# Optimization experiments

Measured on AMD Instinct MI355X. Metric: run time of the kernel, lower is better.

## Reference

```python
import jax, jax.numpy as jnp
import numpy as np
from jax import lax

SUB, NSUB, FRAME, COND, FEAT, PEMB = 40, 4, 160, 256, 20, 64
B, NB_FRAMES = 64, 100
T = NB_FRAMES + 4  # two valid k=3 convs drop 4 frames


def setup_inputs() -> dict:
    keys = iter(jax.random.split(jax.random.key(0), 40))
    def W(shape, fan_in):
        return jax.random.normal(next(keys), shape, jnp.float32) / np.float32(np.sqrt(fan_in))
    z = lambda *s: jnp.zeros(s, jnp.float32)
    inp = {
        'features': jax.random.normal(next(keys), (B, T, FEAT), jnp.float32),
        'period': jax.random.randint(next(keys), (B, T), 32, 256, jnp.int32),
        'nb_frames': NB_FRAMES,
        'rand_shift': jax.random.uniform(next(keys), (B, 1), jnp.float32),
        'pembed': 0.1 * jax.random.normal(next(keys), (256, PEMB), jnp.float32),
        'fd1_w': W((FEAT + PEMB, COND), FEAT + PEMB), 'fd1_b': z(COND),
        'conv1_w': W((COND, COND, 3), 3 * COND), 'conv1_b': z(COND),
        'conv2_w': W((COND, COND, 3), 3 * COND), 'conv2_b': z(COND),
        'fd2_w': W((COND, COND), COND), 'fd2_b': z(COND),
        'sd1_w': W((3 * SUB + COND, COND), 3 * SUB + COND), 'sd1_b': z(COND),
        'sd2_w': W((COND, COND), COND), 'sd2_b': z(COND),
        'g1_wi': W((COND, 3 * COND), COND), 'g1_bi': z(3 * COND),
        'g1_wh': W((COND, 3 * COND), COND), 'g1_bh': z(3 * COND),
        'g2_wi': W((COND, 3 * COND), COND), 'g2_bi': z(3 * COND),
        'g2_wh': W((COND, 3 * COND), COND), 'g2_bh': z(3 * COND),
        'g3_wi': W((COND, 3 * COND), COND), 'g3_bi': z(3 * COND),
        'g3_wh': W((COND, 3 * COND), COND), 'g3_bh': z(3 * COND),
        'out_w': W((COND, SUB), COND), 'out_b': z(SUB),
    }
    return inp


def _gru(x, h, wi, bi, wh, bh):
    # torch GRUCell gate order: r, z, n
    gi = x @ wi + bi
    gh = h @ wh + bh
    i_r, i_z, i_n = jnp.split(gi, 3, axis=1)
    h_r, h_z, h_n = jnp.split(gh, 3, axis=1)
    r = jax.nn.sigmoid(i_r + h_r)
    zt = jax.nn.sigmoid(i_z + h_z)
    n = jnp.tanh(i_n + r * h_n)
    return (1.0 - zt) * n + zt * h


def _conv1d_valid(x, w, b):
    # x: (B, C, T), w: (O, I, 3)
    y = lax.conv_general_dilated(x, w, (1,), 'VALID', dimension_numbers=('NCH', 'OIH', 'NCH'))
    return y + b[None, :, None]


def _forward(features, rand_shift, pembed, fd1_w, fd1_b, conv1_w, conv1_b, conv2_w, conv2_b,
             fd2_w, fd2_b, sd1_w, sd1_b, sd2_w, sd2_b,
             g1_wi, g1_bi, g1_wh, g1_bh, g2_wi, g2_bi, g2_wh, g2_bh, g3_wi, g3_bi, g3_wh, g3_bh,
             out_w, out_b, period, nb_frames):
    b = features.shape[0]
    two_pi = np.float32(2.0 * np.pi)
    # --- phase embedding (gen_phase_embedding on period[:, 3:-1]) ---
    p = period[:, 3:-1].astype(jnp.float32)              # (B, nb_frames)
    w0 = two_pi / p
    w0_shift = jnp.concatenate([two_pi * rand_shift / FRAME, w0[:, :-1]], axis=1)
    cum_phase = FRAME * jnp.cumsum(w0_shift, axis=1)     # (B, nb_frames)
    fine = w0[:, :, None] * jnp.arange(FRAME, dtype=jnp.float32)
    embed = (cum_phase[:, :, None] + fine).reshape(b, nb_frames * NSUB, SUB)
    phase_real = jnp.cos(embed)
    phase_imag = jnp.sin(embed)
    # --- conditioning network ---
    pe = pembed[period]                                  # (B, T, PEMB)
    t = jnp.tanh(jnp.concatenate([features, pe], axis=-1) @ fd1_w + fd1_b)
    x = t.transpose(0, 2, 1)                             # (B, COND, T)
    x = jnp.tanh(_conv1d_valid(x, conv1_w, conv1_b))
    x = jnp.tanh(_conv1d_valid(x, conv2_w, conv2_b))
    cond = jnp.tanh(x.transpose(0, 2, 1) @ fd2_w + fd2_b)  # (B, T-4, COND)
    cond_steps = jnp.repeat(cond[:, :nb_frames], NSUB, axis=1)  # (B, steps, COND)
    xs = (cond_steps.transpose(1, 0, 2), phase_real.transpose(1, 0, 2), phase_imag.transpose(1, 0, 2))
    h0 = jnp.zeros((b, COND), features.dtype)
    prev0 = jnp.zeros((b, SUB), features.dtype)

    def step(carry, inp):
        prev, h1, h2, h3 = carry
        c, pr, pi = inp
        tt = jnp.tanh(jnp.concatenate([c, prev, pr, pi], axis=1) @ sd1_w + sd1_b)
        tt = jnp.tanh(tt @ sd2_w + sd2_b)
        h1 = _gru(tt, h1, g1_wi, g1_bi, g1_wh, g1_bh)
        h2 = _gru(h1, h2, g2_wi, g2_bi, g2_wh, g2_bh)
        h3 = _gru(h2, h3, g3_wi, g3_bi, g3_wh, g3_bh)
        out = jnp.tanh(h3 @ out_w + out_b)
        return (out, h1, h2, h3), out

    (_, h1, h2, h3), outs = lax.scan(step, (prev0, h0, h0, h0), xs)
    sig = outs.transpose(1, 0, 2).reshape(b, -1)         # (B, nb_frames*FRAME)
    return sig, (h1, h2, h3)


def reference(features, period, nb_frames, rand_shift, pembed, fd1_w, fd1_b, conv1_w, conv1_b,
              conv2_w, conv2_b, fd2_w, fd2_b, sd1_w, sd1_b, sd2_w, sd2_b,
              g1_wi, g1_bi, g1_wh, g1_bh, g2_wi, g2_bi, g2_wh, g2_bh, g3_wi, g3_bi, g3_wh, g3_bh,
              out_w, out_b):
    return _forward(features, rand_shift, pembed, fd1_w, fd1_b, conv1_w, conv1_b, conv2_w, conv2_b,
                    fd2_w, fd2_b, sd1_w, sd1_b, sd2_w, sd2_b,
                    g1_wi, g1_bi, g1_wh, g1_bh, g2_wi, g2_bi, g2_wh, g2_bh,
                    g3_wi, g3_bi, g3_wh, g3_bh, out_w, out_b, period, nb_frames)
```

## Files before the change

kernel.cpp:

```cpp
#include <hip/hip_runtime.h>
#include <hip/hip_bf16.h>
#include <math.h>

#define B_ 64
#define T_ 104
#define FEAT_ 20
#define PEMB_ 64
#define COND_ 256
#define SUB_ 40
#define NBF_ 100
#define STEPS_ 400

typedef short short8 __attribute__((ext_vector_type(8)));
typedef float floatx4 __attribute__((ext_vector_type(4)));
typedef unsigned int uintx4 __attribute__((ext_vector_type(4)));

__device__ inline unsigned short f2bf(float x){
  unsigned int u = __float_as_uint(x);
  unsigned int r = (u + 0x7fffu + ((u >> 16) & 1u)) >> 16;
  return (unsigned short)r;
}
__device__ inline float fast_tanh(float x){
  float e = __expf(2.f*x);
  return 1.f - 2.f*__builtin_amdgcn_rcpf(e + 1.f);
}
__device__ inline float fast_sigm(float x){
  return __builtin_amdgcn_rcpf(1.f + __expf(-x));
}
__device__ inline floatx4 mfma16(short8 a, short8 b, floatx4 c){
  return __builtin_amdgcn_mfma_f32_16x16x32_bf16(a, b, c, 0, 0, 0);
}
__device__ inline unsigned long long ld_coh_u64(const unsigned long long* p){
  return __hip_atomic_load(p, __ATOMIC_RELAXED, __HIP_MEMORY_SCOPE_AGENT);
}
__device__ inline void st_coh_u32(unsigned int* p, unsigned int v){
  __hip_atomic_store(p, v, __ATOMIC_RELAXED, __HIP_MEMORY_SCOPE_AGENT);
}

template<int STRIDE, int GCOFF>
__device__ inline void poll_stage(const unsigned int* __restrict__ src, char* dst,
                                  unsigned tgt, int tid){
  int c0 = tid, c1 = tid + 256;
  int r0 = c0 >> 5, g0 = c0 & 31;
  int r1 = c1 >> 5, g1 = c1 & 31;
  const unsigned long long* p0 = (const unsigned long long*)src + (r0*128 + g0*4);
  const unsigned long long* p1 = (const unsigned long long*)src + (r1*128 + g1*4);
  unsigned long long w[8];
  for (;;){
    #pragma unroll
    for (int u = 0; u < 4; ++u) w[u]   = ld_coh_u64(p0 + u);
    #pragma unroll
    for (int u = 0; u < 4; ++u) w[4+u] = ld_coh_u64(p1 + u);
    unsigned mt = 0xFFFFu;
    #pragma unroll
    for (int u = 0; u < 8; ++u){
      unsigned t0 = (unsigned)(w[u] >> 16) & 0xFFFFu;
      unsigned t1 = (unsigned)(w[u] >> 48);
      mt = min(mt, min(t0, t1));
    }
    if (__all((int)(mt >= tgt))) break;
    __builtin_amdgcn_s_sleep(1);
  }
  unsigned int pk0[4], pk1[4];
  #pragma unroll
  for (int u = 0; u < 4; ++u){
    pk0[u] = ((unsigned int)w[u]   & 0xFFFFu) | ((unsigned int)(w[u]   >> 32) << 16);
    pk1[u] = ((unsigned int)w[4+u] & 0xFFFFu) | ((unsigned int)(w[4+u] >> 32) << 16);
  }
  uintx4 v0 = {pk0[0], pk0[1], pk0[2], pk0[3]};
  uintx4 v1 = {pk1[0], pk1[1], pk1[2], pk1[3]};
  *(uintx4*)(dst + (size_t)(r0*STRIDE + ((GCOFF + g0) ^ (r0 & 7)))*16) = v0;
  *(uintx4*)(dst + (size_t)(r1*STRIDE + ((GCOFF + g1) ^ (r1 & 7)))*16) = v1;
}

__global__ void k_phase(const int* __restrict__ period, const float* __restrict__ rshift,
                        float* __restrict__ pr, float* __restrict__ pi){
  int b = blockIdx.x;
  __shared__ float cumf[NBF_], w0f[NBF_];
  if (threadIdx.x == 0){
    double acc = 2.0*M_PI*(double)rshift[b];
    for (int f = 0; f < NBF_; ++f){
      double w0 = 2.0*M_PI/(double)period[b*T_ + 3 + f];
      cumf[f] = (float)fmod(acc, 2.0*M_PI);
      w0f[f] = (float)w0;
      acc += 160.0*w0;
    }
  }
  __syncthreads();
  for (int e = threadIdx.x; e < NBF_*160; e += blockDim.x){
    int f = e/160, j = e - f*160;
    float ph = cumf[f] + w0f[f]*(float)j;
    int s = f*4 + j/40, u = j%40;
    pr[((size_t)b*STEPS_ + s)*SUB_ + u] = cosf(ph);
    pi[((size_t)b*STEPS_ + s)*SUB_ + u] = sinf(ph);
  }
}

__global__ void k_prep(const float* __restrict__ c1w, const float* __restrict__ c2w,
                       float* __restrict__ w1t, float* __restrict__ w2t,
                       unsigned int* __restrict__ msg){
  size_t tid = (size_t)blockIdx.x*blockDim.x + threadIdx.x;
  size_t nt = (size_t)gridDim.x*blockDim.x;
  for (size_t e = tid; e < 131072; e += nt) st_coh_u32(msg + e, 0u);
  for (size_t e = tid; e < 768u*256u; e += nt){
    int kk = (int)(e >> 8), o = (int)(e & 255);
    int i = kk & 255, kc = kk >> 8;
    w1t[e] = c1w[(size_t)o*768 + i*3 + kc];
    w2t[e] = c2w[(size_t)o*768 + i*3 + kc];
  }
}

template<int MODE>
__global__ __launch_bounds__(256) void k_gemm(
    const float* __restrict__ a0, const float* __restrict__ a1, const float* __restrict__ a2,
    const int* __restrict__ ip,
    const float* __restrict__ Bm, const float* __restrict__ bias, float* __restrict__ C)
{
  constexpr int KT = (MODE==0) ? 6 : (MODE==1||MODE==2) ? 48 : (MODE==3) ? 16 : 21;
  __shared__ float As[16][68];
  __shared__ float Bs[16][68];
  int tid = threadIdx.x;
  int m0 = blockIdx.x*64, n0 = blockIdx.y*64;
  int tx = tid & 15, ty = tid >> 4;
  float acc[4][4] = {};
  int am = m0 + (tid >> 2);
  int akq = (tid & 3)*4;
  int bk = tid >> 4;
  int bn4 = (tid & 15)*4;

  for (int kt = 0; kt < KT; ++kt){
    int kbase = kt*16;
    float av[4];
    {
      int k0 = kbase + akq;
      if constexpr (MODE==0){
        if (k0 < 20){
          const float* p = a0 + (size_t)am*FEAT_ + k0;
          #pragma unroll
          for (int u=0;u<4;++u) av[u] = p[u];
        } else if (k0 < 84){
          const float* p = a1 + (size_t)ip[am]*PEMB_ + (k0-20);
          #pragma unroll
          for (int u=0;u<4;++u) av[u] = p[u];
        } else { av[0]=av[1]=av[2]=av[3]=0.f; }
      } else if constexpr (MODE==1){
        int b = am/102, t2 = am - b*102;
        int i = k0 & 255, kc = k0 >> 8;
        const float* p = a0 + ((size_t)(b*T_ + t2 + kc))*COND_ + i;
        #pragma unroll
        for (int u=0;u<4;++u) av[u] = p[u];
      } else if constexpr (MODE==2){
        int b = am/100, t2 = am - b*100;
        int i = k0 & 255, kc = k0 >> 8;
        const float* p = a0 + ((size_t)(b*102 + t2 + kc))*COND_ + i;
        #pragma unroll
        for (int u=0;u<4;++u) av[u] = p[u];
      } else if constexpr (MODE==3){
        const float* p = a0 + (size_t)am*COND_ + k0;
        #pragma unroll
        for (int u=0;u<4;++u) av[u] = p[u];
      } else {
        int b = am/400, s = am - b*400;
        const float* p;
        if (k0 < 256)      p = a0 + ((size_t)(b*100 + (s>>2)))*COND_ + k0;
        else if (k0 < 296) p = a1 + ((size_t)(b*400 + s))*SUB_ + (k0-256);
        else               p = a2 + ((size_t)(b*400 + s))*SUB_ + (k0-296);
        #pragma unroll
        for (int u=0;u<4;++u) av[u] = p[u];
      }
    }
    float bv[4];
    {
      int kB = kbase + bk;
      if constexpr (MODE==0){
        if (kB < 84){
          const float* p = Bm + (size_t)kB*256 + n0 + bn4;
          #pragma unroll
          for (int u=0;u<4;++u) bv[u] = p[u];
        } else { bv[0]=bv[1]=bv[2]=bv[3]=0.f; }
      } else if constexpr (MODE==4){
        int krow = (kB < 256) ? kB : kB + 40;
        const float* p = Bm + (size_t)krow*256 + n0 + bn4;
        #pragma unroll
        for (int u=0;u<4;++u) bv[u] = p[u];
      } else {
        const float* p = Bm + (size_t)kB*256 + n0 + bn4;
        #pragma unroll
        for (int u=0;u<4;++u) bv[u] = p[u];
      }
    }
    #pragma unroll
    for (int u=0;u<4;++u) As[akq+u][tid>>2] = av[u];
    #pragma unroll
    for (int u=0;u<4;++u) Bs[bk][bn4+u] = bv[u];
    __syncthreads();
    #pragma unroll
    for (int k = 0; k < 16; ++k){
      float a4[4], b4[4];
      #pragma unroll
      for (int i=0;i<4;++i) a4[i] = As[k][ty*4+i];
      #pragma unroll
      for (int j=0;j<4;++j) b4[j] = Bs[k][tx*4+j];
      #pragma unroll
      for (int i=0;i<4;++i)
        #pragma unroll
        for (int j=0;j<4;++j)
          acc[i][j] += a4[i]*b4[j];
    }
    __syncthreads();
  }
  #pragma unroll
  for (int i=0;i<4;++i){
    int m = m0 + ty*4 + i;
    #pragma unroll
    for (int j=0;j<4;++j){
      int n = n0 + tx*4 + j;
      float v = acc[i][j] + bias[n];
      if constexpr (MODE == 4){
        int b = m/400, s = m - b*400;
        C[((size_t)s*64 + b)*256 + n] = v;
      } else {
        C[(size_t)m*256 + n] = fast_tanh(v);
      }
    }
  }
}

__global__ __launch_bounds__(256, 1) void k_scan(
  const float* __restrict__ sd1_w, const float* __restrict__ sd2_w, const float* __restrict__ sd2_b,
  const float* __restrict__ g1_wi, const float* __restrict__ g1_bi, const float* __restrict__ g1_wh, const float* __restrict__ g1_bh,
  const float* __restrict__ g2_wi, const float* __restrict__ g2_bi, const float* __restrict__ g2_wh, const float* __restrict__ g2_bh,
  const float* __restrict__ g3_wi, const float* __restrict__ g3_bi, const float* __restrict__ g3_wh, const float* __restrict__ g3_bh,
  const float* __restrict__ out_w, const float* __restrict__ out_b,
  const float* __restrict__ tt1p,
  unsigned int* __restrict__ tt2buf, unsigned int* __restrict__ h1buf,
  unsigned int* __restrict__ h2buf, unsigned int* __restrict__ h3buf,
  float* __restrict__ out)
{
  __shared__ __align__(16) char smem[65536];
  int tid = threadIdx.x;
  int lane = tid & 63, wave = tid >> 6;
  int q = lane >> 4, nI = lane & 15;
  int bI = blockIdx.x;
  int g = bI >> 6, rr = bI & 63;
  int set = rr >> 4, sl = rr & 15;
  int b0 = g*16;

  if (set == 0){
    char* outwF = smem;
    char* sd1p0 = smem + 24576;
    char* sd1p1 = smem + 40960;
    char* sd2F  = smem + 45056;
    char* stage = smem + 53248;
    char* prevl = smem + 61440;
    int col1 = sl*16 + nI;

    for (int t = wave; t < 24; t += 4){
      int nt = t >> 3, kk = t & 7;
      int c = nt*16 + nI;
      unsigned short v[8];
      #pragma unroll
      for (int j = 0; j < 8; ++j){
        int k = kk*32 + q*8 + j;
        v[j] = (c < 40) ? f2bf(out_w[(size_t)k*40 + c]) : (unsigned short)0;
      }
      *(short8*)(outwF + (t*64 + lane)*16) = *(short8*)v;
    }
    for (int t = wave; t < 16; t += 4){
      unsigned short v[8];
      #pragma unroll
      for (int j = 0; j < 8; ++j){
        int k = q*8 + j;
        v[j] = f2bf(sd1_w[(size_t)(256+k)*256 + t*16 + nI]);
      }
      *(short8*)(sd1p0 + (t*64 + lane)*16) = *(short8*)v;
    }
    {
      int nt = tid >> 4, ln = tid & 15;
      unsigned short v[8];
      #pragma unroll
      for (int j = 0; j < 8; ++j)
        v[j] = f2bf(sd1_w[(size_t)(256+32+j)*256 + nt*16 + ln]);
      *(short8*)(sd1p1 + tid*16) = *(short8*)v;
    }
    for (int t = wave; t < 8; t += 4){
      unsigned short v[8];
      #pragma unroll
      for (int j = 0; j < 8; ++j){
        int k = t*32 + q*8 + j;
        v[j] = f2bf(sd2_w[(size_t)k*256 + col1]);
      }
      *(short8*)(sd2F + (t*64 + lane)*16) = *(short8*)v;
    }
    for (int e = tid; e < 16*72; e += 256) *(unsigned short*)(prevl + e*2) = 0;
    float bout = 0.f;
    if (wave < 3){ int c = wave*16 + nI; if (c < 40) bout = out_b[c]; }
    float bsd2 = sd2_b[col1];
    __syncthreads();

    for (int s = 0; s <= STEPS_; ++s){
      float t1r[16];
      if (s < STEPS_){
        const float* tb = tt1p + ((size_t)s*64 + b0)*256;
        #pragma unroll
        for (int ii = 0; ii < 4; ++ii){
          int c = (wave*4 + ii)*16 + nI;
          #pragma unroll
          for (int i = 0; i < 4; ++i)
            t1r[ii*4+i] = tb[(q*4+i)*256 + c];
        }
      }
      if (s > 0){
        const unsigned int* h3s = h3buf + ((size_t)((s+1)&1)*4 + g)*4096;
        poll_stage<32,0>(h3s, stage, (unsigned)s, tid);
        __syncthreads();
        if (wave < 3){
          floatx4 acc = {0.f,0.f,0.f,0.f};
          #pragma unroll
          for (int kk = 0; kk < 8; ++kk){
            short8 a = *(const short8*)(stage + (nI*32 + ((kk*4+q) ^ (nI & 7)))*16);
            short8 b = *(const short8*)(outwF + ((wave*8+kk)*64 + lane)*16);
            acc = mfma16(a, b, acc);
          }
          int c = wave*16 + nI;
          #pragma unroll
          for (int i = 0; i < 4; ++i){
            int row = q*4 + i;
            float pv = (c < 40) ? fast_tanh(acc[i] + bout) : 0.f;
            *(unsigned short*)(prevl + (row*72 + c)*2) = f2bf(pv);
            if (sl == 0 && c < 40)
              out[(size_t)(b0+row)*16000 + (size_t)(s-1)*40 + c] = pv;
          }
        }
      }
      if (s == STEPS_) break;
      __syncthreads();
      #pragma unroll
      for (int ii = 0; ii < 4; ++ii){
        int nt = wave*4 + ii;
        floatx4 acc = {0.f,0.f,0.f,0.f};
        short8 a0v = *(const short8*)(prevl + nI*144 + q*16);
        short8 b0v = *(const short8*)(sd1p0 + (nt*64 + lane)*16);
        acc = mfma16(a0v, b0v, acc);
        short8 a1v = *(const short8*)(prevl + nI*144 + 64 + q*16);
        short8 b1v = {0,0,0,0,0,0,0,0};
        if (q == 0) b1v = *(const short8*)(sd1p1 + (nt*16 + nI)*16);
        acc = mfma16(a1v, b1v, acc);
        int c = nt*16 + nI;
        #pragma unroll
        for (int i = 0; i < 4; ++i){
          int row = q*4 + i;
          float tv = fast_tanh(acc[i] + t1r[ii*4+i]);
          int gc = c >> 3;
          *(unsigned short*)(stage + (row*32 + (gc ^ (row & 7)))*16 + (c & 7)*2) = f2bf(tv);
        }
      }
      __syncthreads();
      if (wave == 0){
        floatx4 acc = {0.f,0.f,0.f,0.f};
        #pragma unroll
        for (int kk = 0; kk < 8; ++kk){
          short8 a = *(const short8*)(stage + (nI*32 + ((kk*4+q) ^ (nI & 7)))*16);
          short8 b = *(const short8*)(sd2F + (kk*64 + lane)*16);
          acc = mfma16(a, b, acc);
        }
        unsigned int* t2 = tt2buf + ((size_t)(s&1)*4 + g)*4096;
        unsigned int tg = (unsigned)(s+1) << 16;
        #pragma unroll
        for (int i = 0; i < 4; ++i){
          int row = q*4 + i;
          st_coh_u32(&t2[row*256 + col1], tg | (unsigned)f2bf(fast_tanh(acc[i] + bsd2)));
        }
      }
      __syncthreads();
    }
  } else {
    int gi_ = set - 1;
    const float* wi = (gi_==0) ? g1_wi : (gi_==1) ? g2_wi : g3_wi;
    const float* wh = (gi_==0) ? g1_wh : (gi_==1) ? g2_wh : g3_wh;
    const float* bi = (gi_==0) ? g1_bi : (gi_==1) ? g2_bi : g3_bi;
    const float* bh = (gi_==0) ? g1_bh : (gi_==1) ? g2_bh : g3_bh;
    unsigned int* hOut = (gi_==0) ? h1buf : (gi_==1) ? h2buf : h3buf;
    const unsigned int* xBase = (gi_==0) ? tt2buf : (gi_==1) ? h1buf : h2buf;
    char* wlds  = smem;
    char* stage = smem + 49152;
    int hc0 = sl*16;

    for (int t = wave; t < 48; t += 4){
      unsigned short v[8];
      #pragma unroll
      for (int j = 0; j < 8; ++j){
        float w;
        if (t < 32){
          int k512 = (t & 15)*32 + q*8 + j;
          int col = ((t < 16) ? 0 : 256) + hc0 + nI;
          w = (k512 < 256) ? wi[(size_t)k512*768 + col] : wh[(size_t)(k512-256)*768 + col];
        } else if (t < 40){
          int k = (t-32)*32 + q*8 + j;
          w = wi[(size_t)k*768 + 512 + hc0 + nI];
        } else {
          int k = (t-40)*32 + q*8 + j;
          w = wh[(size_t)k*768 + 512 + hc0 + nI];
        }
        v[j] = f2bf(w);
      }
      *(short8*)(wlds + (t*64 + lane)*16) = *(short8*)v;
    }
    int erow = tid >> 4, ecol = tid & 15;
    int cg = hc0 + ecol;
    float br  = bi[cg] + bh[cg];
    float bz  = bi[256+cg] + bh[256+cg];
    float bin = bi[512+cg];
    float bhn = bh[512+cg];
    float hstate = 0.f;
    __syncthreads();

    for (int s = 0; s < STEPS_; ++s){
      const unsigned int* hs = hOut + ((size_t)((s+1)&1)*4 + g)*4096;
      poll_stage<64,32>(hs, stage, (unsigned)s, tid);
      __syncthreads();
      floatx4 acc = {0.f,0.f,0.f,0.f};
      if (wave < 2){
        int tb = wave*16;
        #pragma unroll
        for (int kt = 8; kt < 16; ++kt){
          short8 a = *(const short8*)(stage + (nI*64 + ((kt*4+q) ^ (nI & 7)))*16);
          short8 b = *(const short8*)(wlds + ((tb+kt)*64 + lane)*16);
          acc = mfma16(a, b, acc);
        }
      } else if (wave == 3){
        #pragma unroll
        for (int kt = 0; kt < 8; ++kt){
          short8 a = *(const short8*)(stage + (nI*64 + ((32 + kt*4+q) ^ (nI & 7)))*16);
          short8 b = *(const short8*)(wlds + ((40+kt)*64 + lane)*16);
          acc = mfma16(a, b, acc);
        }
      }
      const unsigned int* xs = xBase + ((size_t)(s&1)*4 + g)*4096;
      poll_stage<64,0>(xs, stage, (unsigned)(s+1), tid);
      __syncthreads();
      if (wave < 2){
        int tb = wave*16;
        #pragma unroll
        for (int kt = 0; kt < 8; ++kt){
          short8 a = *(const short8*)(stage + (nI*64 + ((kt*4+q) ^ (nI & 7)))*16);
          short8 b = *(const short8*)(wlds + ((tb+kt)*64 + lane)*16);
          acc = mfma16(a, b, acc);
        }
      } else if (wave == 2){
        #pragma unroll
        for (int kt = 0; kt < 8; ++kt){
          short8 a = *(const short8*)(stage + (nI*64 + ((kt*4+q) ^ (nI & 7)))*16);
          short8 b = *(const short8*)(wlds + ((32+kt)*64 + lane)*16);
          acc = mfma16(a, b, acc);
        }
      }
      __syncthreads();
      float* ex = (float*)stage;
      {
        float* dst = ex + wave*256;
        #pragma unroll
        for (int i = 0; i < 4; ++i) dst[(q*4+i)*16 + nI] = acc[i];
      }
      __syncthreads();
      {
        float rv  = fast_sigm(ex[tid] + br);
        float zv  = fast_sigm(ex[256 + tid] + bz);
        float nv  = fast_tanh(ex[512 + tid] + bin + rv*(ex[768 + tid] + bhn));
        float hv  = (1.f - zv)*nv + zv*hstate;
        hstate = hv;
        unsigned int* ho = hOut + ((size_t)(s&1)*4 + g)*4096;
        st_coh_u32(&ho[erow*256 + cg], ((unsigned)(s+1) << 16) | (unsigned)f2bf(hv));
        if (s == STEPS_-1)
          out[1024000 + gi_*16384 + (size_t)(b0+erow)*256 + cg] = hv;
      }
      __syncthreads();
    }
  }
}

extern "C" void kernel_launch(void* const* d_in, const int* in_sizes, int n_in,
                              void* d_out, int out_size, void* d_ws, size_t ws_size,
                              hipStream_t stream){
  (void)in_sizes; (void)n_in; (void)out_size; (void)ws_size;
  const float* features = (const float*)d_in[0];
  const int*   period   = (const int*)d_in[1];
  const float* rshift   = (const float*)d_in[3];
  const float* pembed   = (const float*)d_in[4];
  const float* fd1_w = (const float*)d_in[5];  const float* fd1_b = (const float*)d_in[6];
  const float* c1w   = (const float*)d_in[7];  const float* c1b   = (const float*)d_in[8];
  const float* c2w   = (const float*)d_in[9];  const float* c2b   = (const float*)d_in[10];
  const float* fd2_w = (const float*)d_in[11]; const float* fd2_b = (const float*)d_in[12];
  const float* sd1_w = (const float*)d_in[13]; const float* sd1_b = (const float*)d_in[14];
  const float* sd2_w = (const float*)d_in[15]; const float* sd2_b = (const float*)d_in[16];
  const float* g1_wi = (const float*)d_in[17]; const float* g1_bi = (const float*)d_in[18];
  const float* g1_wh = (const float*)d_in[19]; const float* g1_bh = (const float*)d_in[20];
  const float* g2_wi = (const float*)d_in[21]; const float* g2_bi = (const float*)d_in[22];
  const float* g2_wh = (const float*)d_in[23]; const float* g2_bh = (const float*)d_in[24];
  const float* g3_wi = (const float*)d_in[25]; const float* g3_bi = (const float*)d_in[26];
  const float* g3_wh = (const float*)d_in[27]; const float* g3_bh = (const float*)d_in[28];
  const float* out_w = (const float*)d_in[29]; const float* out_b = (const float*)d_in[30];

  char* ws = (char*)d_ws;
  size_t off = 0;
  auto alloc = [&](size_t bytes)->char*{
    char* p = ws + off; off += (bytes + 255) & ~(size_t)255; return p;
  };
  unsigned int* msg = (unsigned int*)alloc(524288);
  unsigned int* tt2b = msg;
  unsigned int* h1b  = msg + 32768;
  unsigned int* h2b  = msg + 65536;
  unsigned int* h3b  = msg + 98304;
  float* tt1p = (float*)alloc((size_t)B_*STEPS_*COND_*4);
  float* pr   = (float*)alloc((size_t)B_*STEPS_*SUB_*4);
  float* pi   = (float*)alloc((size_t)B_*STEPS_*SUB_*4);
  float* tbuf = (float*)alloc((size_t)B_*T_*COND_*4);
  float* x1   = (float*)alloc((size_t)B_*102*COND_*4);
  float* x2   = (float*)alloc((size_t)B_*100*COND_*4);
  float* cb   = (float*)alloc((size_t)B_*100*COND_*4);
  float* w1t  = (float*)alloc((size_t)768*256*4);
  float* w2t  = (float*)alloc((size_t)768*256*4);

  k_phase<<<64, 256, 0, stream>>>(period, rshift, pr, pi);
  k_prep<<<256, 256, 0, stream>>>(c1w, c2w, w1t, w2t, msg);
  k_gemm<0><<<dim3(104,4), 256, 0, stream>>>(features, pembed, nullptr, period, fd1_w, fd1_b, tbuf);
  k_gemm<1><<<dim3(102,4), 256, 0, stream>>>(tbuf, nullptr, nullptr, nullptr, w1t, c1b, x1);
  k_gemm<2><<<dim3(100,4), 256, 0, stream>>>(x1, nullptr, nullptr, nullptr, w2t, c2b, x2);
  k_gemm<3><<<dim3(100,4), 256, 0, stream>>>(x2, nullptr, nullptr, nullptr, fd2_w, fd2_b, cb);
  k_gemm<4><<<dim3(400,4), 256, 0, stream>>>(cb, pr, pi, nullptr, sd1_w, sd1_b, tt1p);
  k_scan<<<256, 256, 0, stream>>>(sd1_w, sd2_w, sd2_b,
                                  g1_wi, g1_bi, g1_wh, g1_bh,
                                  g2_wi, g2_bi, g2_wh, g2_bh,
                                  g3_wi, g3_bi, g3_wh, g3_bh,
                                  out_w, out_b, tt1p,
                                  tt2b, h1b, h2b, h3b, (float*)d_out);
}
```

Baseline: 4.506 ms.

## Add XCD-local fast message buffers with coherent fallback for scan inter-block exchange

The scan kernel now launches 512 blocks, and half of them exit straight away so that each batch group's 64 active blocks sit on one XCD, given round-robin block placement modulo 8. Every message is written twice: once with plain volatile stores to a new 'fast' buffer meant to hit the shared XCD-local L2, and once to the old agent-coherent buffer. Polling checks the fast copy first and reads the coherent copy only as a fallback. A global counter barrier makes sure the fast buffers are zeroed before the steps begin. The aim is to cut the latency of cross-block polling in the 400-step recurrence, but this relies on assumptions about how blocks are mapped to XCDs and adds double stores and a startup barrier.

```diff
diff --git a/kernel.cpp b/kernel.cpp
--- a/kernel.cpp
+++ b/kernel.cpp
@@ -33,30 +33,52 @@
 __device__ inline unsigned long long ld_coh_u64(const unsigned long long* p){
   return __hip_atomic_load(p, __ATOMIC_RELAXED, __HIP_MEMORY_SCOPE_AGENT);
 }
+__device__ inline unsigned int ld_coh_u32(const unsigned int* p){
+  return __hip_atomic_load(p, __ATOMIC_RELAXED, __HIP_MEMORY_SCOPE_AGENT);
+}
 __device__ inline void st_coh_u32(unsigned int* p, unsigned int v){
   __hip_atomic_store(p, v, __ATOMIC_RELAXED, __HIP_MEMORY_SCOPE_AGENT);
 }
+__device__ inline void st_fast_u32(unsigned int* p, unsigned int v){
+  *(volatile unsigned int*)p = v;
+}
+__device__ inline unsigned long long ld_fast_u64(const unsigned long long* p){
+  return *(const volatile unsigned long long*)p;
+}
 
 template<int STRIDE, int GCOFF>
-__device__ inline void poll_stage(const unsigned int* __restrict__ src, char* dst,
-                                  unsigned tgt, int tid){
+__device__ inline void xfer(const unsigned int* __restrict__ fsrc,
+                            const unsigned int* __restrict__ ssrc,
+                            char* dst, unsigned tgt, int tid){
   int c0 = tid, c1 = tid + 256;
   int r0 = c0 >> 5, g0 = c0 & 31;
   int r1 = c1 >> 5, g1 = c1 & 31;
-  const unsigned long long* p0 = (const unsigned long long*)src + (r0*128 + g0*4);
-  const unsigned long long* p1 = (const unsigned long long*)src + (r1*128 + g1*4);
+  const unsigned long long* f0 = (const unsigned long long*)fsrc + (r0*128 + g0*4);
+  const unsigned long long* f1 = (const unsigned long long*)fsrc + (r1*128 + g1*4);
+  const unsigned long long* s0 = (const unsigned long long*)ssrc + (r0*128 + g0*4);
+  const unsigned long long* s1 = (const unsigned long long*)ssrc + (r1*128 + g1*4);
   unsigned long long w[8];
   for (;;){
     #pragma unroll
-    for (int u = 0; u < 4; ++u) w[u]   = ld_coh_u64(p0 + u);
-    #pragma unroll
-    for (int u = 0; u < 4; ++u) w[4+u] = ld_coh_u64(p1 + u);
+    for (int u = 0; u < 4; ++u) w[u]   = ld_fast_u64(f0 + u);
+    #pragma unroll
+    for (int u = 0; u < 4; ++u) w[4+u] = ld_fast_u64(f1 + u);
     unsigned mt = 0xFFFFu;
     #pragma unroll
     for (int u = 0; u < 8; ++u){
-      unsigned t0 = (unsigned)(w[u] >> 16) & 0xFFFFu;
-      unsigned t1 = (unsigned)(w[u] >> 48);
-      mt = min(mt, min(t0, t1));
+      mt = min(mt, (unsigned)(w[u] >> 16) & 0xFFFFu);
+      mt = min(mt, (unsigned)(w[u] >> 48));
+    }
+    if (__all((int)(mt >= tgt))) break;
+    #pragma unroll
+    for (int u = 0; u < 4; ++u) w[u]   = ld_coh_u64(s0 + u);
+    #pragma unroll
+    for (int u = 0; u < 4; ++u) w[4+u] = ld_coh_u64(s1 + u);
+    mt = 0xFFFFu;
+    #pragma unroll
+    for (int u = 0; u < 8; ++u){
+      mt = min(mt, (unsigned)(w[u] >> 16) & 0xFFFFu);
+      mt = min(mt, (unsigned)(w[u] >> 48));
     }
     if (__all((int)(mt >= tgt))) break;
     __builtin_amdgcn_s_sleep(1);
@@ -98,10 +120,10 @@
 
 __global__ void k_prep(const float* __restrict__ c1w, const float* __restrict__ c2w,
                        float* __restrict__ w1t, float* __restrict__ w2t,
-                       unsigned int* __restrict__ msg){
+                       unsigned int* __restrict__ coh){
   size_t tid = (size_t)blockIdx.x*blockDim.x + threadIdx.x;
   size_t nt = (size_t)gridDim.x*blockDim.x;
-  for (size_t e = tid; e < 131072; e += nt) st_coh_u32(msg + e, 0u);
+  for (size_t e = tid; e < 131392; e += nt) st_coh_u32(coh + e, 0u);
   for (size_t e = tid; e < 768u*256u; e += nt){
     int kk = (int)(e >> 8), o = (int)(e & 255);
     int i = kk & 255, kc = kk >> 8;
@@ -235,16 +257,43 @@
   const float* __restrict__ tt1p,
   unsigned int* __restrict__ tt2buf, unsigned int* __restrict__ h1buf,
   unsigned int* __restrict__ h2buf, unsigned int* __restrict__ h3buf,
+  unsigned int* __restrict__ tt2F, unsigned int* __restrict__ h1F,
+  unsigned int* __restrict__ h2F, unsigned int* __restrict__ h3F,
+  unsigned int* __restrict__ cnt,
   float* __restrict__ out)
 {
   __shared__ __align__(16) char smem[65536];
+  int bI = blockIdx.x;
+  int cl = bI & 7;
+  if (cl >= 4) return;
+  int g = cl;
+  int inner = bI >> 3;
+  int set = inner >> 4, sl = inner & 15;
   int tid = threadIdx.x;
   int lane = tid & 63, wave = tid >> 6;
   int q = lane >> 4, nI = lane & 15;
-  int bI = blockIdx.x;
-  int g = bI >> 6, rr = bI & 63;
-  int set = rr >> 4, sl = rr & 15;
   int b0 = g*16;
+
+  if (set == 0){
+    for (int e = tid; e < 8192; e += 256){
+      int p = e >> 12;
+      st_fast_u32(h3F + ((size_t)p*4 + g)*4096 + (e & 4095), 0u);
+    }
+  } else {
+    unsigned int* ownF = (set==1) ? h1F : (set==2) ? h2F : h3F;
+    unsigned int* xF   = (set==1) ? tt2F : (set==2) ? h1F : h2F;
+    for (int e = tid; e < 8192; e += 256){
+      int p = e >> 12;
+      st_fast_u32(ownF + ((size_t)p*4 + g)*4096 + (e & 4095), 0u);
+      st_fast_u32(xF   + ((size_t)p*4 + g)*4096 + (e & 4095), 0u);
+    }
+  }
+  __syncthreads();
+  if (tid == 0){
+    __hip_atomic_fetch_add(cnt, 1u, __ATOMIC_RELAXED, __HIP_MEMORY_SCOPE_AGENT);
+    while (ld_coh_u32(cnt) < 256u) __builtin_amdgcn_s_sleep(8);
+  }
+  __syncthreads();
 
   if (set == 0){
     char* outwF = smem;
@@ -311,8 +360,8 @@
         }
       }
       if (s > 0){
-        const unsigned int* h3s = h3buf + ((size_t)((s+1)&1)*4 + g)*4096;
-        poll_stage<32,0>(h3s, stage, (unsigned)s, tid);
+        size_t pb = ((size_t)((s+1)&1)*4 + g)*4096;
+        xfer<32,0>(h3F + pb, h3buf + pb, stage, (unsigned)s, tid);
         __syncthreads();
         if (wave < 3){
           floatx4 acc = {0.f,0.f,0.f,0.f};
@@ -364,12 +413,17 @@
           short8 b = *(const short8*)(sd2F + (kk*64 + lane)*16);
           acc = mfma16(a, b, acc);
         }
-        unsigned int* t2 = tt2buf + ((size_t)(s&1)*4 + g)*4096;
-        unsigned int tg = (unsigned)(s+1) << 16;
+        size_t pb = ((size_t)(s&1)*4 + g)*4096;
+        unsigned int* t2  = tt2buf + pb;
+        unsigned int* t2f = tt2F + pb;
+        unsigned tg = (unsigned)(s+1) << 16;
         #pragma unroll
         for (int i = 0; i < 4; ++i){
           int row = q*4 + i;
-          st_coh_u32(&t2[row*256 + col1], tg | (unsigned)f2bf(fast_tanh(acc[i] + bsd2)));
+          unsigned pw = tg | (unsigned)f2bf(fast_tanh(acc[i] + bsd2));
+          int idx = row*256 + col1;
+          st_fast_u32(t2f + idx, pw);
+          st_coh_u32(t2 + idx, pw);
         }
       }
       __syncthreads();
@@ -380,8 +434,10 @@
     const float* wh = (gi_==0) ? g1_wh : (gi_==1) ? g2_wh : g3_wh;
     const float* bi = (gi_==0) ? g1_bi : (gi_==1) ? g2_bi : g3_bi;
     const float* bh = (gi_==0) ? g1_bh : (gi_==1) ? g2_bh : g3_bh;
-    unsigned int* hOut = (gi_==0) ? h1buf : (gi_==1) ? h2buf : h3buf;
-    const unsigned int* xBase = (gi_==0) ? tt2buf : (gi_==1) ? h1buf : h2buf;
+    unsigned int* hOut  = (gi_==0) ? h1buf : (gi_==1) ? h2buf : h3buf;
+    unsigned int* hOutF = (gi_==0) ? h1F : (gi_==1) ? h2F : h3F;
+    const unsigned int* xBase  = (gi_==0) ? tt2buf : (gi_==1) ? h1buf : h2buf;
+    const unsigned int* xBaseF = (gi_==0) ? tt2F : (gi_==1) ? h1F : h2F;
     char* wlds  = smem;
     char* stage = smem + 49152;
     int hc0 = sl*16;
@@ -416,8 +472,10 @@
     __syncthreads();
 
     for (int s = 0; s < STEPS_; ++s){
-      const unsigned int* hs = hOut + ((size_t)((s+1)&1)*4 + g)*4096;
-      poll_stage<64,32>(hs, stage, (unsigned)s, tid);
+      {
+        size_t pb = ((size_t)((s+1)&1)*4 + g)*4096;
+        xfer<64,32>(hOutF + pb, hOut + pb, stage, (unsigned)s, tid);
+      }
       __syncthreads();
       floatx4 acc = {0.f,0.f,0.f,0.f};
       if (wave < 2){
@@ -436,8 +494,10 @@
           acc = mfma16(a, b, acc);
         }
       }
-      const unsigned int* xs = xBase + ((size_t)(s&1)*4 + g)*4096;
-      poll_stage<64,0>(xs, stage, (unsigned)(s+1), tid);
+      {
+        size_t pb = ((size_t)(s&1)*4 + g)*4096;
+        xfer<64,0>(xBaseF + pb, xBase + pb, stage, (unsigned)(s+1), tid);
+      }
       __syncthreads();
       if (wave < 2){
         int tb = wave*16;
@@ -469,8 +529,11 @@
         float nv  = fast_tanh(ex[512 + tid] + bin + rv*(ex[768 + tid] + bhn));
         float hv  = (1.f - zv)*nv + zv*hstate;
         hstate = hv;
-        unsigned int* ho = hOut + ((size_t)(s&1)*4 + g)*4096;
-        st_coh_u32(&ho[erow*256 + cg], ((unsigned)(s+1) << 16) | (unsigned)f2bf(hv));
+        size_t pb = ((size_t)(s&1)*4 + g)*4096;
+        unsigned pw = ((unsigned)(s+1) << 16) | (unsigned)f2bf(hv);
+        int idx = erow*256 + cg;
+        st_fast_u32(hOutF + pb + idx, pw);
+        st_coh_u32(hOut + pb + idx, pw);
         if (s == STEPS_-1)
           out[1024000 + gi_*16384 + (size_t)(b0+erow)*256 + cg] = hv;
       }
@@ -506,11 +569,17 @@
   auto alloc = [&](size_t bytes)->char*{
     char* p = ws + off; off += (bytes + 255) & ~(size_t)255; return p;
   };
-  unsigned int* msg = (unsigned int*)alloc(524288);
-  unsigned int* tt2b = msg;
-  unsigned int* h1b  = msg + 32768;
-  unsigned int* h2b  = msg + 65536;
-  unsigned int* h3b  = msg + 98304;
+  unsigned int* coh = (unsigned int*)alloc(131392u*4u);
+  unsigned int* tt2b = coh;
+  unsigned int* h1b  = coh + 32768;
+  unsigned int* h2b  = coh + 65536;
+  unsigned int* h3b  = coh + 98304;
+  unsigned int* cnt  = coh + 131072;
+  unsigned int* fastz = (unsigned int*)alloc(131072u*4u);
+  unsigned int* tt2F = fastz;
+  unsigned int* h1F  = fastz + 32768;
+  unsigned int* h2F  = fastz + 65536;
+  unsigned int* h3F  = fastz + 98304;
   float* tt1p = (float*)alloc((size_t)B_*STEPS_*COND_*4);
   float* pr   = (float*)alloc((size_t)B_*STEPS_*SUB_*4);
   float* pi   = (float*)alloc((size_t)B_*STEPS_*SUB_*4);
@@ -522,16 +591,18 @@
   float* w2t  = (float*)alloc((size_t)768*256*4);
 
   k_phase<<<64, 256, 0, stream>>>(period, rshift, pr, pi);
-  k_prep<<<256, 256, 0, stream>>>(c1w, c2w, w1t, w2t, msg);
+  k_prep<<<256, 256, 0, stream>>>(c1w, c2w, w1t, w2t, coh);
   k_gemm<0><<<dim3(104,4), 256, 0, stream>>>(features, pembed, nullptr, period, fd1_w, fd1_b, tbuf);
   k_gemm<1><<<dim3(102,4), 256, 0, stream>>>(tbuf, nullptr, nullptr, nullptr, w1t, c1b, x1);
   k_gemm<2><<<dim3(100,4), 256, 0, stream>>>(x1, nullptr, nullptr, nullptr, w2t, c2b, x2);
   k_gemm<3><<<dim3(100,4), 256, 0, stream>>>(x2, nullptr, nullptr, nullptr, fd2_w, fd2_b, cb);
   k_gemm<4><<<dim3(400,4), 256, 0, stream>>>(cb, pr, pi, nullptr, sd1_w, sd1_b, tt1p);
-  k_scan<<<256, 256, 0, stream>>>(sd1_w, sd2_w, sd2_b,
+  k_scan<<<512, 256, 0, stream>>>(sd1_w, sd2_w, sd2_b,
                                   g1_wi, g1_bi, g1_wh, g1_bh,
                                   g2_wi, g2_bi, g2_wh, g2_bh,
                                   g3_wi, g3_bi, g3_wh, g3_bh,
                                   out_w, out_b, tt1p,
-                                  tt2b, h1b, h2b, h3b, (float*)d_out);
-}
+                                  tt2b, h1b, h2b, h3b,
+                                  tt2F, h1F, h2F, h3F,
+                                  cnt, (float*)d_out);
+}
```

New measurement: 8.667 ms. 92.3% more time.

## Run GRU gate MFMAs and update in one wave, drop LDS exchange and barriers

Applied to the files above, without the earlier changes.

The GRU recurrent loop now has wave 0 compute all four gate accumulators (r, z, input-n, hidden-n) itself and apply the GRU update in registers. This removes the LDS float exchange of partial results and two block barriers per step. The polling loop drops its s_sleep, and the trailing barrier in the sample-rate loop is removed to shorten per-step synchronization latency on the serial critical path. In exchange, one wave does four times the MFMA work while the others only help with staging, and busier polling plus fewer barriers may raise memory contention or risk ordering hazards on the reused stage buffer.

```diff
diff --git a/kernel.cpp b/kernel.cpp
--- a/kernel.cpp
+++ b/kernel.cpp
@@ -38,13 +38,11 @@
 }
 
 template<int STRIDE, int GCOFF>
-__device__ inline void poll_stage(const unsigned int* __restrict__ src, char* dst,
-                                  unsigned tgt, int tid){
-  int c0 = tid, c1 = tid + 256;
-  int r0 = c0 >> 5, g0 = c0 & 31;
-  int r1 = c1 >> 5, g1 = c1 & 31;
+__device__ inline void xfer(const unsigned int* __restrict__ src, char* dst,
+                            unsigned tgt, int tid){
+  int r0 = tid >> 5, g0 = tid & 31;
   const unsigned long long* p0 = (const unsigned long long*)src + (r0*128 + g0*4);
-  const unsigned long long* p1 = (const unsigned long long*)src + (r1*128 + g1*4);
+  const unsigned long long* p1 = p0 + 8*128;
   unsigned long long w[8];
   for (;;){
     #pragma unroll
@@ -54,12 +52,10 @@
     unsigned mt = 0xFFFFu;
     #pragma unroll
     for (int u = 0; u < 8; ++u){
-      unsigned t0 = (unsigned)(w[u] >> 16) & 0xFFFFu;
-      unsigned t1 = (unsigned)(w[u] >> 48);
-      mt = min(mt, min(t0, t1));
+      mt = min(mt, (unsigned)(w[u] >> 16) & 0xFFFFu);
+      mt = min(mt, (unsigned)(w[u] >> 48));
     }
     if (__all((int)(mt >= tgt))) break;
-    __builtin_amdgcn_s_sleep(1);
   }
   unsigned int pk0[4], pk1[4];
   #pragma unroll
@@ -69,8 +65,9 @@
   }
   uintx4 v0 = {pk0[0], pk0[1], pk0[2], pk0[3]};
   uintx4 v1 = {pk1[0], pk1[1], pk1[2], pk1[3]};
+  int r1 = r0 + 8;
   *(uintx4*)(dst + (size_t)(r0*STRIDE + ((GCOFF + g0) ^ (r0 & 7)))*16) = v0;
-  *(uintx4*)(dst + (size_t)(r1*STRIDE + ((GCOFF + g1) ^ (r1 & 7)))*16) = v1;
+  *(uintx4*)(dst + (size_t)(r1*STRIDE + ((GCOFF + g0) ^ (r1 & 7)))*16) = v1;
 }
 
 __global__ void k_phase(const int* __restrict__ period, const float* __restrict__ rshift,
@@ -98,10 +95,10 @@
 
 __global__ void k_prep(const float* __restrict__ c1w, const float* __restrict__ c2w,
                        float* __restrict__ w1t, float* __restrict__ w2t,
-                       unsigned int* __restrict__ msg){
+                       unsigned int* __restrict__ coh){
   size_t tid = (size_t)blockIdx.x*blockDim.x + threadIdx.x;
   size_t nt = (size_t)gridDim.x*blockDim.x;
-  for (size_t e = tid; e < 131072; e += nt) st_coh_u32(msg + e, 0u);
+  for (size_t e = tid; e < 131072; e += nt) st_coh_u32(coh + e, 0u);
   for (size_t e = tid; e < 768u*256u; e += nt){
     int kk = (int)(e >> 8), o = (int)(e & 255);
     int i = kk & 255, kc = kk >> 8;
@@ -312,7 +309,7 @@
       }
       if (s > 0){
         const unsigned int* h3s = h3buf + ((size_t)((s+1)&1)*4 + g)*4096;
-        poll_stage<32,0>(h3s, stage, (unsigned)s, tid);
+        xfer<32,0>(h3s, stage, (unsigned)s, tid);
         __syncthreads();
         if (wave < 3){
           floatx4 acc = {0.f,0.f,0.f,0.f};
@@ -365,14 +362,13 @@
           acc = mfma16(a, b, acc);
         }
         unsigned int* t2 = tt2buf + ((size_t)(s&1)*4 + g)*4096;
-        unsigned int tg = (unsigned)(s+1) << 16;
+        unsigned tg = (unsigned)(s+1) << 16;
         #pragma unroll
         for (int i = 0; i < 4; ++i){
           int row = q*4 + i;
           st_coh_u32(&t2[row*256 + col1], tg | (unsigned)f2bf(fast_tanh(acc[i] + bsd2)));
         }
       }
-      __syncthreads();
     }
   } else {
     int gi_ = set - 1;
@@ -406,75 +402,63 @@
       }
       *(short8*)(wlds + (t*64 + lane)*16) = *(short8*)v;
     }
-    int erow = tid >> 4, ecol = tid & 15;
-    int cg = hc0 + ecol;
+    int cg = hc0 + nI;
     float br  = bi[cg] + bh[cg];
     float bz  = bi[256+cg] + bh[256+cg];
     float bin = bi[512+cg];
     float bhn = bh[512+cg];
-    float hstate = 0.f;
+    floatx4 hst = {0.f,0.f,0.f,0.f};
     __syncthreads();
 
     for (int s = 0; s < STEPS_; ++s){
-      const unsigned int* hs = hOut + ((size_t)((s+1)&1)*4 + g)*4096;
-      poll_stage<64,32>(hs, stage, (unsigned)s, tid);
+      floatx4 ar = {0.f,0.f,0.f,0.f}, az = {0.f,0.f,0.f,0.f};
+      floatx4 ain = {0.f,0.f,0.f,0.f}, ahn = {0.f,0.f,0.f,0.f};
+      {
+        const unsigned int* hs = hOut + ((size_t)((s+1)&1)*4 + g)*4096;
+        xfer<64,32>(hs, stage, (unsigned)s, tid);
+      }
       __syncthreads();
-      floatx4 acc = {0.f,0.f,0.f,0.f};
-      if (wave < 2){
-        int tb = wave*16;
+      if (wave == 0){
         #pragma unroll
         for (int kt = 8; kt < 16; ++kt){
           short8 a = *(const short8*)(stage + (nI*64 + ((kt*4+q) ^ (nI & 7)))*16);
-          short8 b = *(const short8*)(wlds + ((tb+kt)*64 + lane)*16);
-          acc = mfma16(a, b, acc);
-        }
-      } else if (wave == 3){
+          ar = mfma16(a, *(const short8*)(wlds + ((kt)*64 + lane)*16), ar);
+          az = mfma16(a, *(const short8*)(wlds + ((16+kt)*64 + lane)*16), az);
+        }
         #pragma unroll
         for (int kt = 0; kt < 8; ++kt){
           short8 a = *(const short8*)(stage + (nI*64 + ((32 + kt*4+q) ^ (nI & 7)))*16);
-          short8 b = *(const short8*)(wlds + ((40+kt)*64 + lane)*16);
-          acc = mfma16(a, b, acc);
-        }
-      }
-      const unsigned int* xs = xBase + ((size_t)(s&1)*4 + g)*4096;
-      poll_stage<64,0>(xs, stage, (unsigned)(s+1), tid);
+          ahn = mfma16(a, *(const short8*)(wlds + ((40+kt)*64 + lane)*16), ahn);
+        }
+      }
+      {
+        const unsigned int* xs = xBase + ((size_t)(s&1)*4 + g)*4096;
+        xfer<64,0>(xs, stage, (unsigned)(s+1), tid);
+      }
       __syncthreads();
-      if (wave < 2){
-        int tb = wave*16;
+      if (wave == 0){
         #pragma unroll
         for (int kt = 0; kt < 8; ++kt){
           short8 a = *(const short8*)(stage + (nI*64 + ((kt*4+q) ^ (nI & 7)))*16);
-          short8 b = *(const short8*)(wlds + ((tb+kt)*64 + lane)*16);
-          acc = mfma16(a, b, acc);
-        }
-      } else if (wave == 2){
-        #pragma unroll
-        for (int kt = 0; kt < 8; ++kt){
-          short8 a = *(const short8*)(stage + (nI*64 + ((kt*4+q) ^ (nI & 7)))*16);
-          short8 b = *(const short8*)(wlds + ((32+kt)*64 + lane)*16);
-          acc = mfma16(a, b, acc);
-        }
-      }
-      __syncthreads();
-      float* ex = (float*)stage;
-      {
-        float* dst = ex + wave*256;
-        #pragma unroll
-        for (int i = 0; i < 4; ++i) dst[(q*4+i)*16 + nI] = acc[i];
-      }
-      __syncthreads();
-      {
-        float rv  = fast_sigm(ex[tid] + br);
-        float zv  = fast_sigm(ex[256 + tid] + bz);
-        float nv  = fast_tanh(ex[512 + tid] + bin + rv*(ex[768 + tid] + bhn));
-        float hv  = (1.f - zv)*nv + zv*hstate;
-        hstate = hv;
+          ar  = mfma16(a, *(const short8*)(wlds + ((kt)*64 + lane)*16), ar);
+          az  = mfma16(a, *(const short8*)(wlds + ((16+kt)*64 + lane)*16), az);
+          ain = mfma16(a, *(const short8*)(wlds + ((32+kt)*64 + lane)*16), ain);
+        }
         unsigned int* ho = hOut + ((size_t)(s&1)*4 + g)*4096;
-        st_coh_u32(&ho[erow*256 + cg], ((unsigned)(s+1) << 16) | (unsigned)f2bf(hv));
-        if (s == STEPS_-1)
-          out[1024000 + gi_*16384 + (size_t)(b0+erow)*256 + cg] = hv;
-      }
-      __syncthreads();
+        unsigned tg = (unsigned)(s+1) << 16;
+        #pragma unroll
+        for (int i = 0; i < 4; ++i){
+          int row = q*4 + i;
+          float rv = fast_sigm(ar[i] + br);
+          float zv = fast_sigm(az[i] + bz);
+          float nv = fast_tanh(ain[i] + bin + rv*(ahn[i] + bhn));
+          float hv = (1.f - zv)*nv + zv*hst[i];
+          hst[i] = hv;
+          st_coh_u32(&ho[row*256 + cg], tg | (unsigned)f2bf(hv));
+          if (s == STEPS_-1)
+            out[1024000 + gi_*16384 + (size_t)(b0+row)*256 + cg] = hv;
+        }
+      }
     }
   }
 }
```

New measurement: 7.366 ms. +63.5%, slower.
